# Optimization experiments

Measured on AMD Instinct MI355X. Metric: run time of the kernel, lower is better.

## Reference

```python
import jax, jax.numpy as jnp
import numpy as np
import math

HIDDEN = 1024
HEADS = 16

def setup_inputs() -> dict:
    key = jax.random.key(0)
    k1, k2, k3 = jax.random.split(key, 3)
    B, T, C = 4, 2048, HIDDEN
    x = jax.random.normal(k1, (B, T, C), dtype=jnp.float32)
    w_qkv = jax.random.normal(k2, (C, 3 * C), dtype=jnp.float32) * (1.0 / math.sqrt(C))
    b_qkv = jnp.zeros((3 * C,), dtype=jnp.float32)
    w_out = jax.random.normal(k3, (C, C), dtype=jnp.float32) * (1.0 / math.sqrt(C))
    b_out = jnp.zeros((C,), dtype=jnp.float32)
    return {"x": x, "w_qkv": w_qkv, "b_qkv": b_qkv, "w_out": w_out, "b_out": b_out}

def reference(x, w_qkv, b_qkv, w_out, b_out):
    B, T, C = x.shape
    H = HEADS
    D = C // H  # head dim
    qkv = x @ w_qkv + b_qkv  # [B,T,3C]
    q, k, v = jnp.split(qkv, 3, axis=2)
    # [B,T,C] -> [B,H,T,D]
    q = q.reshape(B, T, H, D).transpose(0, 2, 1, 3)
    k = k.reshape(B, T, H, D).transpose(0, 2, 1, 3)
    v = v.reshape(B, T, H, D).transpose(0, 2, 1, 3)
    scale = 1.0 / math.sqrt(D)
    logits = jnp.einsum('bhqd,bhkd->bhqk', q, k) * scale  # [B,H,T,T]
    causal = jnp.tril(jnp.ones((T, T), dtype=bool))
    logits = jnp.where(causal[None, None, :, :], logits, -jnp.inf)
    probs = jax.nn.softmax(logits, axis=-1)
    out = jnp.einsum('bhqk,bhkd->bhqd', probs, v)  # [B,H,T,D]
    out = out.transpose(0, 2, 1, 3).reshape(B, T, C)
    return out @ w_out + b_out
```

## Files before the change

### kernel.cpp

```cpp
#include <hip/hip_runtime.h>
#include <hip/hip_bf16.h>

#define C_DIM  1024
#define NHEAD  16
#define DHEAD  64
#define T_LEN  2048
#define B_SZ   4
#define M_ROWS (B_SZ * T_LEN)
#define QKV_N  (3 * C_DIM)

typedef __bf16 bf16x8 __attribute__((ext_vector_type(8)));
typedef float  f32x4  __attribute__((ext_vector_type(4)));
typedef unsigned short ushort8_t __attribute__((ext_vector_type(8)));
typedef unsigned int   uint4_t   __attribute__((ext_vector_type(4)));

__device__ __forceinline__ unsigned short f2bf(float f) {
    union { float f; unsigned int u; } v; v.f = f;
    unsigned int r = v.u + 0x7FFFu + ((v.u >> 16) & 1u);
    return (unsigned short)(r >> 16);
}

__device__ __forceinline__ bf16x8 as_bf16x8(ushort8_t u) {
    return __builtin_bit_cast(bf16x8, u);
}

__device__ __forceinline__ f32x4 mfma16(bf16x8 a, bf16x8 b, f32x4 c) {
    return __builtin_amdgcn_mfma_f32_16x16x32_bf16(a, b, c, 0, 0, 0);
}

#define GLL16(gsrc, ldst) __builtin_amdgcn_global_load_lds( \
    (const __attribute__((address_space(1))) void*)(gsrc),  \
    (__attribute__((address_space(3))) void*)(ldst), 16, 0, 0)

__device__ __forceinline__ int xcd_remap(int id, int nwg) {
    const int q = nwg >> 3, r = nwg & 7;
    const int xcd = id & 7, off = id >> 3;
    return (xcd < r) ? (xcd * (q + 1) + off) : (r * (q + 1) + (xcd - r) * q + off);
}

__global__ void k_convert(const float* __restrict__ in, unsigned short* __restrict__ out, int n4) {
    int i = blockIdx.x * blockDim.x + threadIdx.x;
    if (i >= n4) return;
    const float4 v = ((const float4*)in)[i];
    unsigned int lo = (unsigned int)f2bf(v.x) | ((unsigned int)f2bf(v.y) << 16);
    unsigned int hi = (unsigned int)f2bf(v.z) | ((unsigned int)f2bf(v.w) << 16);
    ((uint2*)out)[i] = make_uint2(lo, hi);
}

__global__ void k_transpose_bf16(const float* __restrict__ w, unsigned short* __restrict__ wT,
                                 int K, int N) {
    __shared__ float tile[32][33];
    const int n0 = blockIdx.x * 32, k0 = blockIdx.y * 32;
    const int tx = threadIdx.x, ty = threadIdx.y;
    for (int i = 0; i < 32; i += 8)
        tile[ty + i][tx] = w[(size_t)(k0 + ty + i) * N + (n0 + tx)];
    __syncthreads();
    for (int i = 0; i < 32; i += 8)
        wT[(size_t)(n0 + ty + i) * K + (k0 + tx)] = f2bf(tile[tx][ty + i]);
}

__global__ void k_transpose_v(const unsigned short* __restrict__ qkv,
                              unsigned short* __restrict__ vtg) {
    __shared__ unsigned short tile[32][33];
    const int tt = blockIdx.x;
    const int dy = blockIdx.y;
    const int bh = dy >> 1, dtile = dy & 1;
    const int b = bh >> 4, h = bh & 15;
    const int t0 = tt * 32, d0 = dtile * 32;
    const int tx = threadIdx.x, ty = threadIdx.y;
    const unsigned short* src = qkv + (size_t)b * T_LEN * QKV_N + 2 * C_DIM + h * DHEAD + d0;
    for (int i = 0; i < 32; i += 8)
        tile[ty + i][tx] = src[(size_t)(t0 + ty + i) * QKV_N + tx];
    __syncthreads();
    unsigned short* dst = vtg + ((size_t)bh * DHEAD + d0) * T_LEN + t0;
    for (int i = 0; i < 32; i += 8)
        dst[(size_t)(ty + i) * T_LEN + tx] = tile[tx][ty + i];
}

template<int BF16_OUT>
__global__ __launch_bounds__(256) void k_gemm(const unsigned short* __restrict__ A,
                       const unsigned short* __restrict__ Bt,
                       const float* __restrict__ bias,
                       void* __restrict__ C,
                       unsigned short* __restrict__ vtg,
                       int M, int N, int K) {
    __shared__ unsigned short As[128][64];
    __shared__ unsigned short Bs[128][64];

    const int tid  = threadIdx.x;
    const int lane = tid & 63;
    const int wv   = tid >> 6;
    const int wm = wv >> 1, wn = wv & 1;

    const int nwg = gridDim.x * gridDim.y;
    const int wg  = xcd_remap(blockIdx.y * gridDim.x + blockIdx.x, nwg);
    const int bx = wg % gridDim.x, by = wg / gridDim.x;
    const int m0 = by * 128;
    const int n0 = bx * 128;
    const int lr = lane & 15, lg = lane >> 4;

    f32x4 acc[4][4];
#pragma unroll
    for (int i = 0; i < 4; i++)
#pragma unroll
        for (int j = 0; j < 4; j++) acc[i][j] = (f32x4){0.f, 0.f, 0.f, 0.f};

    const int gr = lane >> 3;
    const int gc = 8 * ((lane & 7) ^ gr);

    for (int kt = 0; kt < K; kt += 64) {
        __syncthreads();
#pragma unroll
        for (int j = 0; j < 4; j++) {
            const int row = 32 * wv + 8 * j;
            GLL16(A  + (size_t)(m0 + row + gr) * K + kt + gc, &As[row][0]);
            GLL16(Bt + (size_t)(n0 + row + gr) * K + kt + gc, &Bs[row][0]);
        }
        __syncthreads();

#pragma unroll
        for (int s = 0; s < 2; s++) {
            const int cb = (s * 64 + lg * 16) ^ ((lr & 7) << 4);
            bf16x8 af[4], bfr[4];
#pragma unroll
            for (int i = 0; i < 4; i++)
                af[i] = as_bf16x8(*(const ushort8_t*)((const char*)&As[wm * 64 + i * 16 + lr][0] + cb));
#pragma unroll
            for (int j = 0; j < 4; j++)
                bfr[j] = as_bf16x8(*(const ushort8_t*)((const char*)&Bs[wn * 64 + j * 16 + lr][0] + cb));
#pragma unroll
            for (int i = 0; i < 4; i++)
#pragma unroll
                for (int j = 0; j < 4; j++)
                    acc[i][j] = mfma16(af[i], bfr[j], acc[i][j]);
        }
    }

    const bool isV = (vtg != nullptr) && (n0 >= 2 * C_DIM);
#pragma unroll
    for (int i = 0; i < 4; i++) {
#pragma unroll
        for (int j = 0; j < 4; j++) {
            const int col = n0 + wn * 64 + j * 16 + lr;
            const float bv = bias ? bias[col] : 0.f;
            if (isV) {
                const int dcol = col - 2 * C_DIM;
                const int hh = dcol >> 6, dd = dcol & 63;
                const int row0 = m0 + wm * 64 + i * 16 + lg * 4;
                const int bb = row0 >> 11, t0 = row0 & (T_LEN - 1);
                const unsigned int p0 = (unsigned int)f2bf(acc[i][j][0] + bv)
                                      | ((unsigned int)f2bf(acc[i][j][1] + bv) << 16);
                const unsigned int p1 = (unsigned int)f2bf(acc[i][j][2] + bv)
                                      | ((unsigned int)f2bf(acc[i][j][3] + bv) << 16);
                *(uint2*)&vtg[(((size_t)(bb * 16 + hh)) * 64 + dd) * T_LEN + t0] = make_uint2(p0, p1);
            } else {
#pragma unroll
                for (int r = 0; r < 4; r++) {
                    const int row = m0 + wm * 64 + i * 16 + lg * 4 + r;
                    const float v = acc[i][j][r] + bv;
                    if (BF16_OUT)
                        ((unsigned short*)C)[(size_t)row * N + col] = f2bf(v);
                    else
                        ((float*)C)[(size_t)row * N + col] = v;
                }
            }
        }
    }
}

#define KS_OFF(B_, ROW_) (((B_) << 13) + ((ROW_) << 7))
#define VS_OFF(B_, ROW_) (16384 + ((B_) << 13) + ((ROW_) << 7))
#define SCALE2 0.180336880f
__global__ __launch_bounds__(256, 2) void k_attn(const unsigned short* __restrict__ qkv,
                                                 const unsigned short* __restrict__ vtg,
                                                 unsigned short* __restrict__ out) {
    __shared__ __align__(16) char smem[32768];

    const int blk = xcd_remap(blockIdx.x, B_SZ * NHEAD * 16);
    const int pr = blk & 15;
    const int h  = (blk >> 4) & 15;
    const int b  = blk >> 8;
    const int bh = b * 16 + h;

    const int tid  = threadIdx.x;
    const int lane = tid & 63;
    const int w    = tid >> 6;
    const int lr = lane & 15, lg = lane >> 4;
    const int gr = lane >> 3;
    const int gc = 8 * ((lane & 7) ^ gr);
    const int ra = w * 16;

    const int sA = lr + 32 * (lg & 1);
    const int sB = sA + 16;
    const int fhi = lg >> 1;

    const size_t base = (size_t)b * T_LEN * QKV_N + (size_t)h * DHEAD;
    const unsigned short* Qp = qkv + base;
    const unsigned short* Kp = qkv + base + C_DIM;
    const unsigned short* Vt = vtg + (size_t)bh * DHEAD * T_LEN;

    int buf = 0;
    for (int t = 0; t < 2; t++) {
        const int qt = (t == 0) ? pr : (31 - pr);
        const int qw = qt * 64 + w * 16;
        const int qg = qw + lr;
        const int R  = qt + 1;

        bf16x8 qf[2];
#pragma unroll
        for (int s = 0; s < 2; s++)
            qf[s] = as_bf16x8(*(const ushort8_t*)&Qp[(size_t)(qw + lr) * QKV_N + s * 32 + lg * 8]);

        f32x4 o[4];
#pragma unroll
        for (int f = 0; f < 4; f++) o[f] = (f32x4){0.f, 0.f, 0.f, 0.f};
        float lp = 0.f;

        GLL16(Kp + (size_t)(ra + gr) * QKV_N + gc,          smem + KS_OFF(buf, ra));
        GLL16(Kp + (size_t)(ra + 8 + gr) * QKV_N + gc,      smem + KS_OFF(buf, ra + 8));
        GLL16(Vt + (size_t)(ra + gr) * T_LEN + gc,          smem + VS_OFF(buf, ra));
        GLL16(Vt + (size_t)(ra + 8 + gr) * T_LEN + gc,      smem + VS_OFF(buf, ra + 8));

        for (int r = 0; r < R; ++r) {
            const int kb = r * 64;

            asm volatile("s_waitcnt vmcnt(0)" ::: "memory");
            __builtin_amdgcn_s_barrier();
            __builtin_amdgcn_sched_barrier(0);

            if (r + 1 < R) {
                const int kn = kb + 64;
                GLL16(Kp + (size_t)(kn + ra + gr) * QKV_N + gc,     smem + KS_OFF(buf ^ 1, ra));
                GLL16(Kp + (size_t)(kn + ra + 8 + gr) * QKV_N + gc, smem + KS_OFF(buf ^ 1, ra + 8));
                GLL16(Vt + (size_t)(ra + gr) * T_LEN + kn + gc,     smem + VS_OFF(buf ^ 1, ra));
                GLL16(Vt + (size_t)(ra + 8 + gr) * T_LEN + kn + gc, smem + VS_OFF(buf ^ 1, ra + 8));
            }

            f32x4 s4[4];
            __builtin_amdgcn_s_setprio(1);
#pragma unroll
            for (int f = 0; f < 4; f++) {
                const int row = f * 16 + lr;
                const bf16x8 kf0 = as_bf16x8(*(const ushort8_t*)
                    (smem + KS_OFF(buf, row) + ((lg * 16) ^ ((lr & 7) << 4))));
                const bf16x8 kf1 = as_bf16x8(*(const ushort8_t*)
                    (smem + KS_OFF(buf, row) + ((64 + lg * 16) ^ ((lr & 7) << 4))));
                f32x4 s = (f32x4){0.f, 0.f, 0.f, 0.f};
                s = mfma16(kf0, qf[0], s);
                s = mfma16(kf1, qf[1], s);
                s4[f] = s;
            }
            __builtin_amdgcn_s_setprio(0);

            const bool last = (r == R - 1);
            unsigned int Dk[4][2];
#pragma unroll
            for (int f = 0; f < 4; f++) {
                unsigned short hh[4];
#pragma unroll
                for (int rr = 0; rr < 4; rr++) {
                    float sv = fminf(s4[f][rr] * SCALE2, 72.f);
                    if (last) {
                        const int kg = kb + f * 16 + lg * 4 + rr;
                        if (kg > qg) sv = -1e30f;
                    }
                    const float e = __builtin_amdgcn_exp2f(sv);
                    lp += e;
                    hh[rr] = __builtin_bit_cast(unsigned short, (__bf16)e);
                }
                Dk[f][0] = (unsigned int)hh[0] | ((unsigned int)hh[1] << 16);
                Dk[f][1] = (unsigned int)hh[2] | ((unsigned int)hh[3] << 16);
            }

#pragma unroll
            for (int st = 0; st < 2; st++) {
                const int a0 = __shfl((int)Dk[2 * st][0],     sA, 64);
                const int b0 = __shfl((int)Dk[2 * st + 1][0], sA, 64);
                const int a1 = __shfl((int)Dk[2 * st][1],     sA, 64);
                const int b1 = __shfl((int)Dk[2 * st + 1][1], sA, 64);
                const int a2 = __shfl((int)Dk[2 * st][0],     sB, 64);
                const int b2 = __shfl((int)Dk[2 * st + 1][0], sB, 64);
                const int a3 = __shfl((int)Dk[2 * st][1],     sB, 64);
                const int b3 = __shfl((int)Dk[2 * st + 1][1], sB, 64);
                uint4_t pw;
                pw.x = (unsigned int)(fhi ? b0 : a0);
                pw.y = (unsigned int)(fhi ? b1 : a1);
                pw.z = (unsigned int)(fhi ? b2 : a2);
                pw.w = (unsigned int)(fhi ? b3 : a3);
                const bf16x8 pa = __builtin_bit_cast(bf16x8, pw);

                __builtin_amdgcn_s_setprio(1);
#pragma unroll
                for (int f = 0; f < 4; f++) {
                    const int row = f * 16 + lr;
                    const bf16x8 bv = as_bf16x8(*(const ushort8_t*)
                        (smem + VS_OFF(buf, row) + ((st * 64 + lg * 16) ^ ((lr & 7) << 4))));
                    o[f] = mfma16(pa, bv, o[f]);
                }
                __builtin_amdgcn_s_setprio(0);
            }

            buf ^= 1;
        }

        lp += __shfl_xor(lp, 16, 64);
        lp += __shfl_xor(lp, 32, 64);

        float inv[4];
#pragma unroll
        for (int rr = 0; rr < 4; rr++)
            inv[rr] = 1.f / __shfl(lp, lg * 4 + rr, 64);
#pragma unroll
        for (int rr = 0; rr < 4; rr++) {
            const int q = qw + lg * 4 + rr;
#pragma unroll
            for (int f = 0; f < 4; f++)
                out[((size_t)b * T_LEN + q) * C_DIM + h * DHEAD + f * 16 + lr] =
                    f2bf(o[f][rr] * inv[rr]);
        }
    }
}

extern "C" void kernel_launch(void* const* d_in, const int* in_sizes, int n_in,
                              void* d_out, int out_size, void* d_ws, size_t ws_size,
                              hipStream_t stream) {
    const float* x      = (const float*)d_in[0];
    const float* w_qkv  = (const float*)d_in[1];
    const float* b_qkv  = (const float*)d_in[2];
    const float* w_out  = (const float*)d_in[3];
    const float* b_out  = (const float*)d_in[4];
    float* out = (float*)d_out;

    char* ws = (char*)d_ws;
    unsigned short* xb    = (unsigned short*)(ws);
    unsigned short* wqkvT = (unsigned short*)(ws + 16777216);
    unsigned short* woutT = (unsigned short*)(ws + 16777216 + 6291456);
    unsigned short* qkv   = (unsigned short*)(ws + 25165824);
    unsigned short* attn  = (unsigned short*)(ws + 75497472);

    const size_t VTG_OFF = 92274688ull;
    const bool fused_vt = (ws_size >= VTG_OFF + 16777216ull);
    unsigned short* vtg = fused_vt ? (unsigned short*)(ws + VTG_OFF)
                                   : (unsigned short*)(ws);

    {
        const int n4 = M_ROWS * C_DIM / 4;
        k_convert<<<(n4 + 255) / 256, 256, 0, stream>>>(x, xb, n4);
    }
    k_transpose_bf16<<<dim3(QKV_N / 32, C_DIM / 32), dim3(32, 8), 0, stream>>>(w_qkv, wqkvT, C_DIM, QKV_N);
    k_transpose_bf16<<<dim3(C_DIM / 32, C_DIM / 32), dim3(32, 8), 0, stream>>>(w_out, woutT, C_DIM, C_DIM);
    k_gemm<1><<<dim3(QKV_N / 128, M_ROWS / 128), 256, 0, stream>>>(
        xb, wqkvT, b_qkv, qkv, fused_vt ? vtg : nullptr, M_ROWS, QKV_N, C_DIM);
    if (!fused_vt)
        k_transpose_v<<<dim3(T_LEN / 32, 64 * 2), dim3(32, 8), 0, stream>>>(qkv, vtg);
    k_attn<<<B_SZ * NHEAD * 16, 256, 0, stream>>>(qkv, vtg, attn);
    k_gemm<0><<<dim3(C_DIM / 128, M_ROWS / 128), 256, 0, stream>>>(
        attn, woutT, b_out, out, nullptr, M_ROWS, C_DIM, C_DIM);
}
```

Before: 172.9 us.

## Compute PV as O^T with 16x16x16 MFMA to drop P shuffles

The P·V product is restructured so the exponentiated score fragments, already in the accumulator layout of the QK^T MFMA, feed directly as the B operand of a 16x16x16 bf16 MFMA, with V^T read from LDS as the A operand. This removes the eight cross-lane shuffles per step that converted P into the A-operand layout, and the row-sum broadcast in the epilogue. In exchange it issues twice as many smaller MFMAs, each doing half the K-depth, plus narrower 8-byte LDS reads, and the output store becomes a transposed scatter. If the x16 builtin is unavailable, a fallback pads operands into the 32-deep MFMA.

```diff
diff --git a/kernel.cpp b/kernel.cpp
--- a/kernel.cpp
+++ b/kernel.cpp
@@ -13,6 +13,13 @@
 typedef float  f32x4  __attribute__((ext_vector_type(4)));
 typedef unsigned short ushort8_t __attribute__((ext_vector_type(8)));
 typedef unsigned int   uint4_t   __attribute__((ext_vector_type(4)));
+typedef short          short4_t  __attribute__((ext_vector_type(4)));
+
+#if __has_builtin(__builtin_amdgcn_mfma_f32_16x16x16bf16_1k)
+#define HAVE_MFMA_X16 1
+#else
+#define HAVE_MFMA_X16 0
+#endif
 
 __device__ __forceinline__ unsigned short f2bf(float f) {
     union { float f; unsigned int u; } v; v.f = f;
@@ -190,10 +197,6 @@
     const int gc = 8 * ((lane & 7) ^ gr);
     const int ra = w * 16;
 
-    const int sA = lr + 32 * (lg & 1);
-    const int sB = sA + 16;
-    const int fhi = lg >> 1;
-
     const size_t base = (size_t)b * T_LEN * QKV_N + (size_t)h * DHEAD;
     const unsigned short* Qp = qkv + base;
     const unsigned short* Kp = qkv + base + C_DIM;
@@ -253,7 +256,7 @@
             __builtin_amdgcn_s_setprio(0);
 
             const bool last = (r == R - 1);
-            unsigned int Dk[4][2];
+            unsigned int pb[4][2];
 #pragma unroll
             for (int f = 0; f < 4; f++) {
                 unsigned short hh[4];
@@ -268,56 +271,53 @@
                     lp += e;
                     hh[rr] = __builtin_bit_cast(unsigned short, (__bf16)e);
                 }
-                Dk[f][0] = (unsigned int)hh[0] | ((unsigned int)hh[1] << 16);
-                Dk[f][1] = (unsigned int)hh[2] | ((unsigned int)hh[3] << 16);
-            }
-
-#pragma unroll
-            for (int st = 0; st < 2; st++) {
-                const int a0 = __shfl((int)Dk[2 * st][0],     sA, 64);
-                const int b0 = __shfl((int)Dk[2 * st + 1][0], sA, 64);
-                const int a1 = __shfl((int)Dk[2 * st][1],     sA, 64);
-                const int b1 = __shfl((int)Dk[2 * st + 1][1], sA, 64);
-                const int a2 = __shfl((int)Dk[2 * st][0],     sB, 64);
-                const int b2 = __shfl((int)Dk[2 * st + 1][0], sB, 64);
-                const int a3 = __shfl((int)Dk[2 * st][1],     sB, 64);
-                const int b3 = __shfl((int)Dk[2 * st + 1][1], sB, 64);
+                pb[f][0] = (unsigned int)hh[0] | ((unsigned int)hh[1] << 16);
+                pb[f][1] = (unsigned int)hh[2] | ((unsigned int)hh[3] << 16);
+            }
+
+            __builtin_amdgcn_s_setprio(1);
+#pragma unroll
+            for (int kg = 0; kg < 4; kg++) {
+#if HAVE_MFMA_X16
+                const short4_t pbv = __builtin_bit_cast(short4_t,
+                    make_uint2(pb[kg][0], pb[kg][1]));
+#else
                 uint4_t pw;
-                pw.x = (unsigned int)(fhi ? b0 : a0);
-                pw.y = (unsigned int)(fhi ? b1 : a1);
-                pw.z = (unsigned int)(fhi ? b2 : a2);
-                pw.w = (unsigned int)(fhi ? b3 : a3);
-                const bf16x8 pa = __builtin_bit_cast(bf16x8, pw);
-
-                __builtin_amdgcn_s_setprio(1);
-#pragma unroll
-                for (int f = 0; f < 4; f++) {
-                    const int row = f * 16 + lr;
-                    const bf16x8 bv = as_bf16x8(*(const ushort8_t*)
-                        (smem + VS_OFF(buf, row) + ((st * 64 + lg * 16) ^ ((lr & 7) << 4))));
-                    o[f] = mfma16(pa, bv, o[f]);
+                pw.x = pb[kg][0]; pw.y = pb[kg][1]; pw.z = 0u; pw.w = 0u;
+                const bf16x8 pbv8 = __builtin_bit_cast(bf16x8, pw);
+#endif
+#pragma unroll
+                for (int fd = 0; fd < 4; fd++) {
+                    const int drow = fd * 16 + lr;
+                    const uint2 va = *(const uint2*)(smem + VS_OFF(buf, drow) +
+                                     ((kg * 32 + lg * 8) ^ ((lr & 7) << 4)));
+#if HAVE_MFMA_X16
+                    o[fd] = __builtin_amdgcn_mfma_f32_16x16x16bf16_1k(
+                        __builtin_bit_cast(short4_t, va), pbv, o[fd], 0, 0, 0);
+#else
+                    uint4_t vw;
+                    vw.x = va.x; vw.y = va.y; vw.z = va.x; vw.w = va.y;
+                    o[fd] = mfma16(__builtin_bit_cast(bf16x8, vw), pbv8, o[fd]);
+#endif
                 }
-                __builtin_amdgcn_s_setprio(0);
-            }
+            }
+            __builtin_amdgcn_s_setprio(0);
 
             buf ^= 1;
         }
 
         lp += __shfl_xor(lp, 16, 64);
         lp += __shfl_xor(lp, 32, 64);
-
-        float inv[4];
-#pragma unroll
-        for (int rr = 0; rr < 4; rr++)
-            inv[rr] = 1.f / __shfl(lp, lg * 4 + rr, 64);
-#pragma unroll
-        for (int rr = 0; rr < 4; rr++) {
-            const int q = qw + lg * 4 + rr;
-#pragma unroll
-            for (int f = 0; f < 4; f++)
-                out[((size_t)b * T_LEN + q) * C_DIM + h * DHEAD + f * 16 + lr] =
-                    f2bf(o[f][rr] * inv[rr]);
-        }
+        const float inv = 1.f / lp;
+
+#pragma unroll
+        for (int fd = 0; fd < 4; fd++)
+#pragma unroll
+            for (int rr = 0; rr < 4; rr++) {
+                const int d = fd * 16 + lg * 4 + rr;
+                out[((size_t)b * T_LEN + qw + lr) * C_DIM + h * DHEAD + d] =
+                    f2bf(o[fd][rr] * inv);
+            }
     }
 }
 
```

Measured after the change: 169.5 us. 1.02x faster.
